# Kernel tuning notes

Measured on AMD Instinct MI355X. Metric: run time of the kernel, lower is better.

Reference implementation:

```python
import jax, jax.numpy as jnp
import numpy as np


def setup_inputs() -> dict:
    key = jax.random.key(0)
    ks = jax.random.split(key, 4)
    B, L, E = 2, 2048, 512
    scale = 0.02
    return {
        "x": jax.random.normal(ks[0], (B, L, E), dtype=jnp.float32),
        "Wq": jax.random.normal(ks[1], (E, E), dtype=jnp.float32) * scale,
        "bq": jnp.zeros((E,), dtype=jnp.float32),
        "Wk": jax.random.normal(ks[2], (E, E), dtype=jnp.float32) * scale,
        "bk": jnp.zeros((E,), dtype=jnp.float32),
        "Wv": jax.random.normal(ks[3], (E, E), dtype=jnp.float32) * scale,
        "bv": jnp.zeros((E,), dtype=jnp.float32),
        "window_size": 64,
    }


def reference(x, Wq, bq, Wk, bk, Wv, bv, window_size):
    # x: [B, L, E]; Linear weights stored torch-style as [out, in].
    B, L, E = x.shape
    q = jnp.einsum("ble,fe->blf", x, Wq) + bq  # [B, L, E]
    k = jnp.einsum("ble,fe->blf", x, Wk) + bk
    v = jnp.einsum("ble,fe->blf", x, Wv) + bv

    w = window_size
    W = 2 * w + 1
    # Window indices per query position i: [i-w, i+w], clipped; invalid masked.
    offsets = jnp.arange(-w, w + 1)                 # [W]
    idx = jnp.arange(L)[:, None] + offsets[None, :]  # [L, W]
    valid = (idx >= 0) & (idx < L)                   # [L, W]
    idx_c = jnp.clip(idx, 0, L - 1)

    k_win = k[:, idx_c]  # [B, L, W, E]
    v_win = v[:, idx_c]  # [B, L, W, E]

    scores = jnp.einsum("ble,blwe->blw", q, k_win) / jnp.sqrt(jnp.float32(E))
    scores = jnp.where(valid[None, :, :], scores, -jnp.inf)
    probs = jax.nn.softmax(scores, axis=-1)          # [B, L, W]
    out = jnp.einsum("blw,blwe->ble", probs, v_win)  # [B, L, E]
    return out
```

## Files before the change

### kernel.cpp

```cpp
#include <hip/hip_runtime.h>
#include <cstdint>
#include <cstddef>

#define L_SEQ 2048
#define E_DIM 512
#define B_SZ 2
#define WIN 64
#define SCALE_QK 0.044194173824159216f

typedef __attribute__((ext_vector_type(8))) short short8;
typedef __attribute__((ext_vector_type(4))) float floatx4;

__device__ __forceinline__ unsigned short f2bf(float f) {
    unsigned int u = __float_as_uint(f);
    u += 0x7FFFu + ((u >> 16) & 1u);
    return (unsigned short)(u >> 16);
}

__global__ __launch_bounds__(256) void cvt_kernel(
    const float* __restrict__ x, const float* __restrict__ wq,
    const float* __restrict__ wk, const float* __restrict__ wv,
    unsigned short* __restrict__ xb, unsigned short* __restrict__ wb)
{
    long i = (long)blockIdx.x * 256 + threadIdx.x;
    const float* src;
    unsigned short* dst;
    long off;
    if (i < 524288) {
        src = x; dst = xb; off = i;
    } else {
        long j = i - 524288;
        int w = (int)(j >> 16);
        off = j & 65535;
        src = (w == 0) ? wq : ((w == 1) ? wk : wv);
        dst = wb + (long)w * 262144;
    }
    float4 f = ((const float4*)src)[off];
    ushort4 o;
    o.x = f2bf(f.x); o.y = f2bf(f.y); o.z = f2bf(f.z); o.w = f2bf(f.w);
    ((ushort4*)dst)[off] = o;
}

#define ALD 72
__global__ __launch_bounds__(256) void qkv_gemm(
    const unsigned short* __restrict__ xb,
    const unsigned short* __restrict__ wb,
    const float* __restrict__ bq, const float* __restrict__ bk, const float* __restrict__ bv,
    unsigned short* __restrict__ q, unsigned short* __restrict__ k,
    unsigned short* __restrict__ vt)
{
    __shared__ __align__(16) unsigned short As[64 * ALD];
    __shared__ __align__(16) unsigned short Bs[64 * ALD];

    const int t = threadIdx.x;
    const int w = t >> 6, l = t & 63;
    const int m0 = blockIdx.x * 64, n0 = blockIdx.y * 64, z = blockIdx.z;
    const unsigned short* W = wb + (size_t)z * 262144;
    const float* bias = (z == 0) ? bq : ((z == 1) ? bk : bv);

    floatx4 acc[2][2] = {};
    const int wm = (w >> 1) * 32, wn = (w & 1) * 32;
    const int fr = l & 15, fq = l >> 4, fk = fq * 8;

    const int srow = t >> 2, scol = (t & 3) * 16;
    const unsigned short* gA = xb + (size_t)(m0 + srow) * 512 + scol;
    const unsigned short* gB = W  + (size_t)(n0 + srow) * 512 + scol;

    uint4 ra0 = *(const uint4*)(gA);     uint4 ra1 = *(const uint4*)(gA + 8);
    uint4 rb0 = *(const uint4*)(gB);     uint4 rb1 = *(const uint4*)(gB + 8);

    for (int it = 0; it < 8; it++) {
        *(uint4*)&As[srow * ALD + scol]     = ra0;
        *(uint4*)&As[srow * ALD + scol + 8] = ra1;
        *(uint4*)&Bs[srow * ALD + scol]     = rb0;
        *(uint4*)&Bs[srow * ALD + scol + 8] = rb1;
        __syncthreads();
        if (it < 7) {
            int kk = (it + 1) * 64;
            ra0 = *(const uint4*)(gA + kk); ra1 = *(const uint4*)(gA + kk + 8);
            rb0 = *(const uint4*)(gB + kk); rb1 = *(const uint4*)(gB + kk + 8);
        }
        short8 a[2][2], bf[2][2];
#pragma unroll
        for (int i = 0; i < 2; i++)
#pragma unroll
            for (int kh = 0; kh < 2; kh++)
                a[i][kh] = *(const short8*)&As[(wm + i * 16 + fr) * ALD + kh * 32 + fk];
#pragma unroll
        for (int j = 0; j < 2; j++)
#pragma unroll
            for (int kh = 0; kh < 2; kh++)
                bf[j][kh] = *(const short8*)&Bs[(wn + j * 16 + fr) * ALD + kh * 32 + fk];
#pragma unroll
        for (int kh = 0; kh < 2; kh++)
#pragma unroll
            for (int i = 0; i < 2; i++)
#pragma unroll
                for (int j = 0; j < 2; j++)
                    acc[i][j] = __builtin_amdgcn_mfma_f32_16x16x32_bf16(a[i][kh], bf[j][kh], acc[i][j], 0, 0, 0);
        __syncthreads();
    }

    unsigned short* Tl = As;
    float bv_[2];
#pragma unroll
    for (int j = 0; j < 2; j++) bv_[j] = bias[n0 + wn + j * 16 + fr];

    if (z < 2) {
#pragma unroll
        for (int i = 0; i < 2; i++)
#pragma unroll
            for (int j = 0; j < 2; j++)
#pragma unroll
                for (int r = 0; r < 4; r++)
                    Tl[(wm + i * 16 + fq * 4 + r) * ALD + wn + j * 16 + fr] =
                        f2bf(acc[i][j][r] + bv_[j]);
    } else {
#pragma unroll
        for (int i = 0; i < 2; i++)
#pragma unroll
            for (int j = 0; j < 2; j++)
#pragma unroll
                for (int r = 0; r < 4; r++)
                    Tl[(wn + j * 16 + fr) * ALD + wm + i * 16 + fq * 4 + r] =
                        f2bf(acc[i][j][r] + bv_[j]);
    }
    __syncthreads();

    const int tr = t >> 2, tc = (t & 3) * 16;
    uint4 v0 = *(const uint4*)&Tl[tr * ALD + tc];
    uint4 v1 = *(const uint4*)&Tl[tr * ALD + tc + 8];
    if (z < 2) {
        unsigned short* out = (z == 0) ? q : k;
        *(uint4*)&out[(size_t)(m0 + tr) * 512 + n0 + tc]     = v0;
        *(uint4*)&out[(size_t)(m0 + tr) * 512 + n0 + tc + 8] = v1;
    } else {
        *(uint4*)&vt[(size_t)(n0 + tr) * 4096 + m0 + tc]     = v0;
        *(uint4*)&vt[(size_t)(n0 + tr) * 4096 + m0 + tc + 8] = v1;
    }
}

__global__ __launch_bounds__(64) void scores_kernel(
    const unsigned short* __restrict__ qb, const unsigned short* __restrict__ kb,
    float* __restrict__ S)
{
    const int l = threadIdx.x;
    const int fr = l & 15, fq = l >> 4;
    const int Q0 = blockIdx.x * 16;
    const int nt = blockIdx.y;
    const int b  = blockIdx.z;
    const int R0 = Q0 - WIN;
    const int tok = R0 + nt * 16 + fr;
    const bool kvalid = (tok >= 0) && (tok < L_SEQ);

    const unsigned short* qrow = qb + (size_t)(b * L_SEQ + Q0 + fr) * 512 + fq * 8;
    const unsigned short* krow = kb + (size_t)(b * L_SEQ) * 512 + (size_t)tok * 512 + fq * 8;

    floatx4 acc = {};
#pragma unroll
    for (int ks = 0; ks < 16; ks++) {
        short8 a = *(const short8*)(qrow + ks * 32);
        short8 bfr = {};
        if (kvalid) bfr = *(const short8*)(krow + ks * 32);
        acc = __builtin_amdgcn_mfma_f32_16x16x32_bf16(a, bfr, acc, 0, 0, 0);
    }

    const int jg = nt * 16 + fr;
    float* Srow = S + (size_t)(b * L_SEQ + Q0) * 160 + jg;
#pragma unroll
    for (int r = 0; r < 4; r++) {
        int qq = fq * 4 + r;
        bool valid = (jg >= qq) && (jg <= qq + 128) && kvalid;
        Srow[(size_t)qq * 160] = valid ? acc[r] * SCALE_QK : -1e30f;
    }
}

__global__ __launch_bounds__(64) void pv_kernel(
    const float* __restrict__ S, const unsigned short* __restrict__ vt,
    float* __restrict__ out)
{
    const int l = threadIdx.x;
    const int fr = l & 15, fq = l >> 4;
    const int Q0 = blockIdx.x * 16;
    const int EC = blockIdx.y * 64;
    const int b  = blockIdx.z;
    const int R0 = Q0 - WIN;

    const float* Srow = S + (size_t)(b * L_SEQ + Q0 + fr) * 160 + fq * 8;
    float sv[5][8];
#pragma unroll
    for (int ks = 0; ks < 5; ks++) {
        float4 u0 = *(const float4*)(Srow + ks * 32);
        float4 u1 = *(const float4*)(Srow + ks * 32 + 4);
        sv[ks][0] = u0.x; sv[ks][1] = u0.y; sv[ks][2] = u0.z; sv[ks][3] = u0.w;
        sv[ks][4] = u1.x; sv[ks][5] = u1.y; sv[ks][6] = u1.z; sv[ks][7] = u1.w;
    }
    if (fq >= 2) {
#pragma unroll
        for (int j = 0; j < 8; j++) sv[4][j] = -1e30f;
    }
    float m = -1e30f;
#pragma unroll
    for (int ks = 0; ks < 5; ks++)
#pragma unroll
        for (int j = 0; j < 8; j++) m = fmaxf(m, sv[ks][j]);
    m = fmaxf(m, __shfl_xor(m, 16));
    m = fmaxf(m, __shfl_xor(m, 32));
    float sum = 0.f;
#pragma unroll
    for (int ks = 0; ks < 5; ks++)
#pragma unroll
        for (int j = 0; j < 8; j++) { float e = __expf(sv[ks][j] - m); sv[ks][j] = e; sum += e; }
    sum += __shfl_xor(sum, 16);
    sum += __shfl_xor(sum, 32);
    float inv = 1.f / sum;

    short8 a[5];
#pragma unroll
    for (int ks = 0; ks < 5; ks++)
#pragma unroll
        for (int j = 0; j < 8; j++) a[ks][j] = (short)f2bf(sv[ks][j] * inv);

    floatx4 oa[4] = {};
#pragma unroll
    for (int ks = 0; ks < 5; ks++) {
        int tok0 = R0 + ks * 32 + fq * 8;
        bool tv = (tok0 >= 0) && (tok0 < L_SEQ);
#pragma unroll
        for (int et = 0; et < 4; et++) {
            short8 bfr = {};
            if (tv) bfr = *(const short8*)&vt[(size_t)(EC + et * 16 + fr) * 4096 + b * L_SEQ + tok0];
            oa[et] = __builtin_amdgcn_mfma_f32_16x16x32_bf16(a[ks], bfr, oa[et], 0, 0, 0);
        }
    }

    float* op = out + (size_t)b * L_SEQ * E_DIM;
#pragma unroll
    for (int et = 0; et < 4; et++)
#pragma unroll
        for (int r = 0; r < 4; r++)
            op[(size_t)(Q0 + fq * 4 + r) * 512 + EC + et * 16 + fr] = oa[et][r];
}

extern "C" void kernel_launch(void* const* d_in, const int* in_sizes, int n_in,
                              void* d_out, int out_size, void* d_ws, size_t ws_size,
                              hipStream_t stream)
{
    const float* x  = (const float*)d_in[0];
    const float* Wq = (const float*)d_in[1];
    const float* bq = (const float*)d_in[2];
    const float* Wk = (const float*)d_in[3];
    const float* bk = (const float*)d_in[4];
    const float* Wv = (const float*)d_in[5];
    const float* bv = (const float*)d_in[6];
    float* out = (float*)d_out;

    char* ws = (char*)d_ws;
    unsigned short* qb = (unsigned short*)(ws);
    unsigned short* kb = (unsigned short*)(ws + 4194304);
    unsigned short* vt = (unsigned short*)(ws + 8388608);
    unsigned short* xb = (unsigned short*)(ws + 12582912);
    unsigned short* wb = (unsigned short*)(ws + 16777216);
    float*          S  = (float*)(ws + 18350080);

    cvt_kernel<<<2816, 256, 0, stream>>>(x, Wq, Wk, Wv, xb, wb);
    qkv_gemm<<<dim3(64, 8, 3), 256, 0, stream>>>(xb, wb, bq, bk, bv, qb, kb, vt);
    scores_kernel<<<dim3(128, 9, 2), 64, 0, stream>>>(qb, kb, S);
    pv_kernel<<<dim3(128, 8, 2), 64, 0, stream>>>(S, vt, out);
}
```

Baseline: 112.5 us.

## Fuse windowed scores and softmax-PV into a single attention kernel

Merges the separate scores and PV kernels into one kernel per 16-query tile and batch. Scores for all 9 key tiles are kept in shared memory instead of a global S buffer, Q fragments are held in registers, and the block loops over all output column groups. This removes a kernel launch and the global round trip of the score matrix. In exchange the grid shrinks to 256 single-wave blocks, which greatly cuts parallelism and latency hiding.

Measured after the change: 161.7 us. 43.6% more time.

```diff
diff --git a/kernel.cpp b/kernel.cpp
--- a/kernel.cpp
+++ b/kernel.cpp
@@ -140,53 +140,48 @@
     }
 }
 
-__global__ __launch_bounds__(64) void scores_kernel(
+#define SLD 164
+__global__ __launch_bounds__(64) void attn_fused(
     const unsigned short* __restrict__ qb, const unsigned short* __restrict__ kb,
-    float* __restrict__ S)
-{
+    const unsigned short* __restrict__ vt, float* __restrict__ out)
+{
+    __shared__ __align__(16) float Sl[16 * SLD];
+
     const int l = threadIdx.x;
     const int fr = l & 15, fq = l >> 4;
     const int Q0 = blockIdx.x * 16;
-    const int nt = blockIdx.y;
-    const int b  = blockIdx.z;
+    const int b  = blockIdx.y;
     const int R0 = Q0 - WIN;
-    const int tok = R0 + nt * 16 + fr;
-    const bool kvalid = (tok >= 0) && (tok < L_SEQ);
 
     const unsigned short* qrow = qb + (size_t)(b * L_SEQ + Q0 + fr) * 512 + fq * 8;
-    const unsigned short* krow = kb + (size_t)(b * L_SEQ) * 512 + (size_t)tok * 512 + fq * 8;
-
-    floatx4 acc = {};
-#pragma unroll
-    for (int ks = 0; ks < 16; ks++) {
-        short8 a = *(const short8*)(qrow + ks * 32);
-        short8 bfr = {};
-        if (kvalid) bfr = *(const short8*)(krow + ks * 32);
-        acc = __builtin_amdgcn_mfma_f32_16x16x32_bf16(a, bfr, acc, 0, 0, 0);
-    }
-
-    const int jg = nt * 16 + fr;
-    float* Srow = S + (size_t)(b * L_SEQ + Q0) * 160 + jg;
-#pragma unroll
-    for (int r = 0; r < 4; r++) {
-        int qq = fq * 4 + r;
-        bool valid = (jg >= qq) && (jg <= qq + 128) && kvalid;
-        Srow[(size_t)qq * 160] = valid ? acc[r] * SCALE_QK : -1e30f;
-    }
-}
-
-__global__ __launch_bounds__(64) void pv_kernel(
-    const float* __restrict__ S, const unsigned short* __restrict__ vt,
-    float* __restrict__ out)
-{
-    const int l = threadIdx.x;
-    const int fr = l & 15, fq = l >> 4;
-    const int Q0 = blockIdx.x * 16;
-    const int EC = blockIdx.y * 64;
-    const int b  = blockIdx.z;
-    const int R0 = Q0 - WIN;
-
-    const float* Srow = S + (size_t)(b * L_SEQ + Q0 + fr) * 160 + fq * 8;
+    short8 qf[16];
+#pragma unroll
+    for (int ks = 0; ks < 16; ks++) qf[ks] = *(const short8*)(qrow + ks * 32);
+
+#pragma unroll
+    for (int nt = 0; nt < 9; nt++) {
+        const int tok = R0 + nt * 16 + fr;
+        const bool kvalid = (tok >= 0) && (tok < L_SEQ);
+        const unsigned short* krow = kb + (size_t)(b * L_SEQ) * 512 + (size_t)tok * 512 + fq * 8;
+
+        floatx4 acc = {};
+#pragma unroll
+        for (int ks = 0; ks < 16; ks++) {
+            short8 bfr = {};
+            if (kvalid) bfr = *(const short8*)(krow + ks * 32);
+            acc = __builtin_amdgcn_mfma_f32_16x16x32_bf16(qf[ks], bfr, acc, 0, 0, 0);
+        }
+        const int jg = nt * 16 + fr;
+#pragma unroll
+        for (int r = 0; r < 4; r++) {
+            int qq = fq * 4 + r;
+            bool valid = kvalid && (jg >= qq) && (jg <= qq + 128);
+            Sl[qq * SLD + jg] = valid ? acc[r] * SCALE_QK : -1e30f;
+        }
+    }
+    __syncthreads();
+
+    const float* Srow = &Sl[fr * SLD + fq * 8];
     float sv[5][8];
 #pragma unroll
     for (int ks = 0; ks < 5; ks++) {
@@ -221,25 +216,27 @@
 #pragma unroll
         for (int j = 0; j < 8; j++) a[ks][j] = (short)f2bf(sv[ks][j] * inv);
 
-    floatx4 oa[4] = {};
-#pragma unroll
-    for (int ks = 0; ks < 5; ks++) {
-        int tok0 = R0 + ks * 32 + fq * 8;
-        bool tv = (tok0 >= 0) && (tok0 < L_SEQ);
-#pragma unroll
-        for (int et = 0; et < 4; et++) {
-            short8 bfr = {};
-            if (tv) bfr = *(const short8*)&vt[(size_t)(EC + et * 16 + fr) * 4096 + b * L_SEQ + tok0];
-            oa[et] = __builtin_amdgcn_mfma_f32_16x16x32_bf16(a[ks], bfr, oa[et], 0, 0, 0);
-        }
-    }
-
     float* op = out + (size_t)b * L_SEQ * E_DIM;
 #pragma unroll
-    for (int et = 0; et < 4; et++)
-#pragma unroll
-        for (int r = 0; r < 4; r++)
-            op[(size_t)(Q0 + fq * 4 + r) * 512 + EC + et * 16 + fr] = oa[et][r];
+    for (int eg = 0; eg < 4; eg++) {
+        floatx4 oa[8] = {};
+#pragma unroll
+        for (int ks = 0; ks < 5; ks++) {
+            int tok0 = R0 + ks * 32 + fq * 8;
+            bool tv = (tok0 >= 0) && (tok0 < L_SEQ);
+#pragma unroll
+            for (int e8 = 0; e8 < 8; e8++) {
+                short8 bfr = {};
+                if (tv) bfr = *(const short8*)&vt[(size_t)(eg * 128 + e8 * 16 + fr) * 4096 + b * L_SEQ + tok0];
+                oa[e8] = __builtin_amdgcn_mfma_f32_16x16x32_bf16(a[ks], bfr, oa[e8], 0, 0, 0);
+            }
+        }
+#pragma unroll
+        for (int e8 = 0; e8 < 8; e8++)
+#pragma unroll
+            for (int r = 0; r < 4; r++)
+                op[(size_t)(Q0 + fq * 4 + r) * 512 + eg * 128 + e8 * 16 + fr] = oa[e8][r];
+    }
 }
 
 extern "C" void kernel_launch(void* const* d_in, const int* in_sizes, int n_in,
@@ -261,10 +258,8 @@
     unsigned short* vt = (unsigned short*)(ws + 8388608);
     unsigned short* xb = (unsigned short*)(ws + 12582912);
     unsigned short* wb = (unsigned short*)(ws + 16777216);
-    float*          S  = (float*)(ws + 18350080);
 
     cvt_kernel<<<2816, 256, 0, stream>>>(x, Wq, Wk, Wv, xb, wb);
     qkv_gemm<<<dim3(64, 8, 3), 256, 0, stream>>>(xb, wb, bq, bk, bv, qb, kb, vt);
-    scores_kernel<<<dim3(128, 9, 2), 64, 0, stream>>>(qb, kb, S);
-    pv_kernel<<<dim3(128, 8, 2), 64, 0, stream>>>(S, vt, out);
-}
+    attn_fused<<<dim3(128, 2), 64, 0, stream>>>(qb, kb, vt, out);
+}
```
